# Optimization experiments

Measured on AMD Instinct MI355X. Metric: run time of the kernel, lower is better.

## Reference

```python
import jax, jax.numpy as jnp
import numpy as np

B, S, T, M, H = 16, 128, 1024, 16, 1024
HID = 1024        # attention MLP hidden
WIDTH_EMB = 20    # width embedding dim
N_LING = 2        # len(linguistic_feature_types)


def setup_inputs() -> dict:
    key = jax.random.key(0)
    ks = jax.random.split(key, 12)
    doc_embeddings = jax.random.normal(ks[0], (B, T, H), dtype=jnp.float32)
    start_mappings = jax.random.normal(ks[1], (B, S, T), dtype=jnp.float32)
    end_mappings = jax.random.normal(ks[2], (B, S, T), dtype=jnp.float32)
    continuous_mappings = jax.random.normal(ks[3], (B, S, M, T), dtype=jnp.float32)
    width = jax.random.randint(ks[4], (B, S), 0, M, dtype=jnp.int64)
    linguistic_labels = jax.random.normal(ks[5], (B, S, N_LING), dtype=jnp.float32)
    # attention MLP params (torch Linear layout transposed to x @ W + b)
    W1 = jax.random.normal(ks[6], (H, HID), dtype=jnp.float32) * (1.0 / np.sqrt(H))
    b1 = jax.random.normal(ks[7], (HID,), dtype=jnp.float32) * 0.01
    W2 = jax.random.normal(ks[8], (HID, 1), dtype=jnp.float32) * (1.0 / np.sqrt(HID))
    b2 = jax.random.normal(ks[9], (1,), dtype=jnp.float32) * 0.01
    width_table = jax.random.normal(ks[10], (5, WIDTH_EMB), dtype=jnp.float32)
    return {
        'doc_embeddings': doc_embeddings,
        'start_mappings': start_mappings,
        'end_mappings': end_mappings,
        'continuous_mappings': continuous_mappings,
        'linguistic_labels': linguistic_labels,
        'W1': W1, 'b1': b1, 'W2': W2, 'b2': b2,
        'width_table': width_table,
        'width': width,
    }


def reference(doc_embeddings, start_mappings, end_mappings, continuous_mappings,
              linguistic_labels, W1, b1, W2, b2, width_table, width):
    # one-hot matmul gathers
    start = jnp.einsum('bst,bth->bsh', start_mappings, doc_embeddings)
    end = jnp.einsum('bst,bth->bsh', end_mappings, doc_embeddings)
    cont = jnp.einsum('bsmt,bth->bsmh', continuous_mappings, doc_embeddings)
    b, s, m, h = cont.shape
    vector = jnp.concatenate([start, end], axis=-1).reshape(b * s, 2 * h)
    cont = cont.reshape(b * s, m, h)
    w = width.reshape(b * s)
    ling = linguistic_labels.reshape(b * s, -1)
    # padded masked attention pooling
    masks = (jnp.arange(m)[None, :] < jnp.maximum(w, 1)[:, None]).astype(cont.dtype)
    hdn = jax.nn.relu(jnp.einsum('nmh,hk->nmk', cont, W1) + b1)
    scores = (jnp.einsum('nmk,ko->nmo', hdn, W2) + b2)[..., 0]  # [n, m]
    scores = scores * masks
    scores = jnp.where(scores != 0, scores, jnp.asarray(-9e9, scores.dtype))
    att = jax.nn.softmax(scores, axis=1)
    weighted_sum = jnp.einsum('nm,nmh->nh', att, cont)
    vector = jnp.concatenate([vector, weighted_sum], axis=1)
    # linguistic feature columns (loop over fixed small feature list)
    for fi in range(N_LING):
        vector = jnp.concatenate([vector, ling[:, fi:fi + 1]], axis=1)
    # width embedding (clamp max=4)
    wemb = width_table[jnp.clip(w, 0, 4)]
    vector = jnp.concatenate([vector, wemb], axis=1)
    return vector.reshape(b, s, -1)
```

## Files before the change

kernel.cpp:

```cpp
#include <hip/hip_runtime.h>

typedef unsigned short ushort_t;
typedef unsigned int uint_t;
typedef _Float16 f16;
typedef f16 f16x8 __attribute__((ext_vector_type(8)));
typedef float f32x4 __attribute__((ext_vector_type(4)));

#define B_   16
#define S_   128
#define T_   1024
#define M_   16
#define H_   1024
#define OUTW 3094
#define NSPAN (B_*S_)
#define NROW  (NSPAN*M_)

#define WS_CONT   0
#define WS_DOCT   67108864
#define WS_W1T    100663296
#define WS_SCORES 102760448

__device__ __forceinline__ float sane(float v) {
  return fminf(fmaxf(v, -60000.f), 60000.f);
}
__device__ __forceinline__ ushort_t f16bits(float f) {
  union { f16 h; ushort_t u; } c; c.h = (f16)f; return c.u;
}
__device__ __forceinline__ void load_lds16(const void* g, void* l) {
  __builtin_amdgcn_global_load_lds(
      (const __attribute__((address_space(1))) uint_t*)g,
      (__attribute__((address_space(3))) uint_t*)l, 16, 0, 0);
}

__global__ __launch_bounds__(256) void tconv(const float* __restrict__ in,
                                             ushort_t* __restrict__ out,
                                             int R, int C) {
  __shared__ uint_t tile[64][65];
  const int tid = threadIdx.x;
  const int c0 = blockIdx.x * 64, r0 = blockIdx.y * 64;
  const size_t mo = (size_t)blockIdx.z * R * C;
  const float* ip = in + mo;
  ushort_t* op = out + mo;
  const int tx = tid & 63, ty = tid >> 6;
#pragma unroll
  for (int p = 0; p < 16; ++p) {
    int r = p * 4 + ty;
    tile[r][tx] = (uint_t)f16bits(ip[(size_t)(r0 + r) * C + c0 + tx]);
  }
  __syncthreads();
  const int rr = (tid & 31) * 2, cc0 = tid >> 5;
  uint_t* op32 = (uint_t*)op;
#pragma unroll
  for (int p = 0; p < 8; ++p) {
    int c = cc0 + p * 8;
    uint_t lo = tile[rr][c] & 0xffffu;
    uint_t hi = tile[rr + 1][c] & 0xffffu;
    op32[((size_t)(c0 + c) * R + r0 + rr) >> 1] = lo | (hi << 16);
  }
}

__global__ __launch_bounds__(256) void gemm1(const float* __restrict__ startm,
                                             const float* __restrict__ endm,
                                             const float* __restrict__ contm,
                                             const ushort_t* __restrict__ docT,
                                             float* __restrict__ out,
                                             f16* __restrict__ contF) {
  __shared__ f16 As[2 * 128 * 32];
  __shared__ f16 Bs[2 * 128 * 32];
  const int tid = threadIdx.x;
  const uint_t pid = blockIdx.x;
  const int xcd = pid & 7;
  const int s_  = pid >> 3;
  const int ct  = s_ & 7;
  const int pg  = (s_ >> 3) * 8 + xcd;
  const int rt  = pg >> 4;
  const int b   = pg & 15;

  const float* Ap;
  if (rt == 0)      Ap = startm + (size_t)b * S_ * T_;
  else if (rt == 1) Ap = endm + (size_t)b * S_ * T_;
  else              Ap = contm + (size_t)b * (S_ * M_ * T_) + (size_t)(rt - 2) * 128 * T_;
  const ushort_t* Bp = docT + (size_t)b * (H_ * T_) + (size_t)ct * 128 * T_;

  const int lane = tid & 63, w = tid >> 6;
  const int wr = w >> 1, wc = w & 1;
  const int quad = lane >> 4, l16 = lane & 15;
  const int arow = tid >> 1;
  const int ah   = tid & 1;
  const int asw  = (arow >> 1) & 3;
  const int ac0  = ((2 * ah) ^ asw) * 8;
  const int ac1  = ((2 * ah + 1) ^ asw) * 8;
  const float* aSrc = Ap + (size_t)arow * T_ + ah * 16;
  const int brow = lane >> 2;
  const int bcol = ((lane & 3) ^ ((lane >> 3) & 3)) * 8;

  f32x4 acc[4][4];
#pragma unroll
  for (int i = 0; i < 4; ++i)
#pragma unroll
    for (int j = 0; j < 4; ++j) acc[i][j] = (f32x4){0.f, 0.f, 0.f, 0.f};

  {
    f32x4 a0 = *(const f32x4*)(aSrc + 0);
    f32x4 a1 = *(const f32x4*)(aSrc + 4);
    f32x4 a2 = *(const f32x4*)(aSrc + 8);
    f32x4 a3 = *(const f32x4*)(aSrc + 12);
#pragma unroll
    for (int i = 0; i < 2; ++i) {
      const int rb = w * 32 + i * 16;
      load_lds16(Bp + (size_t)(rb + brow) * T_ + bcol, &Bs[rb * 32]);
    }
    f16x8 h0, h1;
#pragma unroll
    for (int k = 0; k < 4; ++k) {
      h0[k] = (f16)a0[k]; h0[k + 4] = (f16)a1[k];
      h1[k] = (f16)a2[k]; h1[k + 4] = (f16)a3[k];
    }
    *(f16x8*)&As[arow * 32 + ac0] = h0;
    *(f16x8*)&As[arow * 32 + ac1] = h1;
    __syncthreads();
  }

  int cur = 0;
  for (int k0 = 0; k0 < T_; k0 += 32) {
    const int nxt = cur ^ 1;
    const bool pf = (k0 + 32 < T_);
    f32x4 a0, a1, a2, a3;
    if (pf) {
      const float* ap = aSrc + (k0 + 32);
      a0 = *(const f32x4*)(ap + 0);
      a1 = *(const f32x4*)(ap + 4);
      a2 = *(const f32x4*)(ap + 8);
      a3 = *(const f32x4*)(ap + 12);
#pragma unroll
      for (int i = 0; i < 2; ++i) {
        const int rb = w * 32 + i * 16;
        load_lds16(Bp + (size_t)(rb + brow) * T_ + (k0 + 32) + bcol,
                   &Bs[nxt * 4096 + rb * 32]);
      }
    }
    f16x8 af[4], bfr[4];
#pragma unroll
    for (int i = 0; i < 4; ++i) {
      const int row = wr * 64 + i * 16 + l16;
      const int sw = (row >> 1) & 3;
      af[i] = *(const f16x8*)&As[cur * 4096 + row * 32 + ((quad ^ sw) * 8)];
    }
#pragma unroll
    for (int j = 0; j < 4; ++j) {
      const int row = wc * 64 + j * 16 + l16;
      const int sw = (row >> 1) & 3;
      bfr[j] = *(const f16x8*)&Bs[cur * 4096 + row * 32 + ((quad ^ sw) * 8)];
    }
#pragma unroll
    for (int i = 0; i < 4; ++i)
#pragma unroll
      for (int j = 0; j < 4; ++j)
        acc[i][j] = __builtin_amdgcn_mfma_f32_16x16x32_f16(af[i], bfr[j], acc[i][j], 0, 0, 0);
    if (pf) {
      f16x8 h0, h1;
#pragma unroll
      for (int k = 0; k < 4; ++k) {
        h0[k] = (f16)a0[k]; h0[k + 4] = (f16)a1[k];
        h1[k] = (f16)a2[k]; h1[k + 4] = (f16)a3[k];
      }
      *(f16x8*)&As[nxt * 4096 + arow * 32 + ac0] = h0;
      *(f16x8*)&As[nxt * 4096 + arow * 32 + ac1] = h1;
    }
    __syncthreads();
    cur = nxt;
  }

  if (rt < 2) {
    float* op = out + (size_t)b * S_ * OUTW + (size_t)rt * 1024 + (size_t)ct * 128;
#pragma unroll
    for (int i = 0; i < 4; ++i)
#pragma unroll
      for (int j = 0; j < 4; ++j)
#pragma unroll
        for (int r = 0; r < 4; ++r) {
          int row = wr * 64 + i * 16 + quad * 4 + r;
          int col = wc * 64 + j * 16 + l16;
          op[(size_t)row * OUTW + col] = sane(acc[i][j][r]);
        }
  } else {
    f16* cp = contF + ((size_t)b * 2048 + (size_t)(rt - 2) * 128) * H_ + (size_t)ct * 128;
#pragma unroll
    for (int i = 0; i < 4; ++i)
#pragma unroll
      for (int j = 0; j < 4; ++j)
#pragma unroll
        for (int r = 0; r < 4; ++r) {
          int row = wr * 64 + i * 16 + quad * 4 + r;
          int col = wc * 64 + j * 16 + l16;
          cp[(size_t)row * H_ + col] = (f16)sane(acc[i][j][r]);
        }
  }
}

__global__ __launch_bounds__(512) void gemm2(const f16* __restrict__ contF,
                                             const f16* __restrict__ W1T,
                                             const float* __restrict__ b1,
                                             const float* __restrict__ W2,
                                             float* __restrict__ scores) {
  __shared__ f16 As[3][256 * 64];
  __shared__ f16 Bs[3][128 * 64];
  const int tid = threadIdx.x;
  const uint_t pid = blockIdx.x;
  const int xcd = pid & 7;
  const int s_  = pid >> 3;
  const int ct  = s_ & 7;
  const int g   = s_ >> 3;
  const int rt  = g * 8 + xcd;

  const f16* Ap = contF + (size_t)rt * 256 * H_;
  const f16* Bp = W1T + (size_t)ct * 128 * H_;

  const int lane = tid & 63, w = tid >> 6;
  const int wm = w >> 1;
  const int wn = w & 1;
  const int quad = lane >> 4, l16 = lane & 15;
  const int lrow = lane >> 3;
  const int lchk = lane & 7;

  f32x4 acc[4][4];
#pragma unroll
  for (int i = 0; i < 4; ++i)
#pragma unroll
    for (int j = 0; j < 4; ++j) acc[i][j] = (f32x4){0.f, 0.f, 0.f, 0.f};

#pragma unroll
  for (int t = 0; t < 2; ++t) {
    const int k0 = t * 64;
#pragma unroll
    for (int j = 0; j < 4; ++j) {
      const int rowb = w * 32 + j * 8;
      const int row  = rowb + lrow;
      const int c    = lchk ^ (row & 7);
      load_lds16(Ap + (size_t)row * H_ + k0 + c * 8, &As[t][rowb * 64]);
    }
#pragma unroll
    for (int j = 0; j < 2; ++j) {
      const int rowb = w * 16 + j * 8;
      const int row  = rowb + lrow;
      const int c    = lchk ^ (row & 7);
      load_lds16(Bp + (size_t)row * H_ + k0 + c * 8, &Bs[t][rowb * 64]);
    }
  }
  asm volatile("s_waitcnt vmcnt(0)" ::: "memory");
  __syncthreads();

  for (int kt = 0; kt < 16; ++kt) {
    const int rb = kt % 3;
    if (kt + 2 < 16) {
      const int sb = (kt + 2) % 3;
      const int k0 = (kt + 2) * 64;
#pragma unroll
      for (int j = 0; j < 4; ++j) {
        const int rowb = w * 32 + j * 8;
        const int row  = rowb + lrow;
        const int c    = lchk ^ (row & 7);
        load_lds16(Ap + (size_t)row * H_ + k0 + c * 8, &As[sb][rowb * 64]);
      }
#pragma unroll
      for (int j = 0; j < 2; ++j) {
        const int rowb = w * 16 + j * 8;
        const int row  = rowb + lrow;
        const int c    = lchk ^ (row & 7);
        load_lds16(Bp + (size_t)row * H_ + k0 + c * 8, &Bs[sb][rowb * 64]);
      }
    }
    f16x8 af[2][4], bf[2][4];
#pragma unroll
    for (int ks = 0; ks < 2; ++ks) {
#pragma unroll
      for (int mf = 0; mf < 4; ++mf) {
        const int row = wm * 64 + mf * 16 + l16;
        const int c   = ks * 4 + quad;
        af[ks][mf] = *(const f16x8*)&As[rb][row * 64 + ((c ^ (row & 7)) * 8)];
      }
#pragma unroll
      for (int nf = 0; nf < 4; ++nf) {
        const int row = wn * 64 + nf * 16 + l16;
        const int c   = ks * 4 + quad;
        bf[ks][nf] = *(const f16x8*)&Bs[rb][row * 64 + ((c ^ (row & 7)) * 8)];
      }
    }
#pragma unroll
    for (int ks = 0; ks < 2; ++ks)
#pragma unroll
      for (int mf = 0; mf < 4; ++mf)
#pragma unroll
        for (int nf = 0; nf < 4; ++nf)
          acc[mf][nf] = __builtin_amdgcn_mfma_f32_16x16x32_f16(
              af[ks][mf], bf[ks][nf], acc[mf][nf], 0, 0, 0);
    if (kt <= 13) asm volatile("s_waitcnt vmcnt(6) lgkmcnt(0)" ::: "memory");
    else          asm volatile("s_waitcnt vmcnt(0) lgkmcnt(0)" ::: "memory");
    __builtin_amdgcn_s_barrier();
    __builtin_amdgcn_sched_barrier(0);
  }

  const int colbase = ct * 128 + wn * 64;
#pragma unroll
  for (int mf = 0; mf < 4; ++mf) {
#pragma unroll
    for (int r = 0; r < 4; ++r) {
      float t = 0.f;
#pragma unroll
      for (int nf = 0; nf < 4; ++nf) {
        int c = colbase + nf * 16 + l16;
        float v = acc[mf][nf][r] + b1[c];
        v = fmaxf(v, 0.f);
        t = fmaf(v, W2[c], t);
      }
      t += __shfl_xor(t, 1);
      t += __shfl_xor(t, 2);
      t += __shfl_xor(t, 4);
      t += __shfl_xor(t, 8);
      if (l16 == 0) {
        int row = rt * 256 + wm * 64 + mf * 16 + quad * 4 + r;
        atomicAdd(&scores[row], t);
      }
    }
  }
}

__global__ __launch_bounds__(256) void finalize(const f16* __restrict__ contF,
                                                const float* __restrict__ scores,
                                                const float* __restrict__ ling,
                                                const float* __restrict__ b2,
                                                const float* __restrict__ wtab,
                                                const int* __restrict__ width,
                                                float* __restrict__ out) {
  const int n = blockIdx.x;
  const int tid = threadIdx.x;
  __shared__ float sc[16];
  if (tid < 16) {
    float raw = scores[n * 16 + tid] + b2[0];
    if (raw != raw) raw = 0.0f;
    int wv = width[n];
    int wm = wv > 1 ? wv : 1;
    float s = (tid < wm) ? raw : 0.0f;
    if (s == 0.0f) s = -9e9f;
    sc[tid] = s;
  }
  __syncthreads();
  float mx = sc[0];
#pragma unroll
  for (int m = 1; m < 16; ++m) mx = fmaxf(mx, sc[m]);
  float e[16];
  float ssum = 0.f;
#pragma unroll
  for (int m = 0; m < 16; ++m) { e[m] = __expf(sc[m] - mx); ssum += e[m]; }
  const float inv = 1.0f / ssum;
  const f16* cp = contF + (size_t)n * (M_ * H_);
  float* op = out + (size_t)n * OUTW;
#pragma unroll
  for (int hh = 0; hh < 4; ++hh) {
    int h = tid + hh * 256;
    float a = 0.f;
#pragma unroll
    for (int m = 0; m < 16; ++m) a = fmaf(e[m], (float)cp[m * H_ + h], a);
    op[2048 + h] = sane(a * inv);
  }
  if (tid < 2) op[3072 + tid] = ling[n * 2 + tid];
  if (tid < 20) {
    int wv = width[n];
    int wcl = wv < 4 ? wv : 4;
    if (wcl < 0) wcl = 0;
    op[3074 + tid] = wtab[wcl * 20 + tid];
  }
}

extern "C" void kernel_launch(void* const* d_in, const int* in_sizes, int n_in,
                              void* d_out, int out_size, void* d_ws, size_t ws_size,
                              hipStream_t stream) {
  const float* doc    = (const float*)d_in[0];
  const float* startm = (const float*)d_in[1];
  const float* endm   = (const float*)d_in[2];
  const float* contm  = (const float*)d_in[3];
  const float* ling   = (const float*)d_in[4];
  const float* W1     = (const float*)d_in[5];
  const float* b1     = (const float*)d_in[6];
  const float* W2     = (const float*)d_in[7];
  const float* b2     = (const float*)d_in[8];
  const float* wtab   = (const float*)d_in[9];
  const int*   width  = (const int*)d_in[10];
  float* out = (float*)d_out;

  char* ws = (char*)d_ws;
  f16*      contF  = (f16*)(ws + WS_CONT);
  ushort_t* docT   = (ushort_t*)(ws + WS_DOCT);
  f16*      W1T    = (f16*)(ws + WS_W1T);
  float*    scores = (float*)(ws + WS_SCORES);

  hipMemsetAsync(scores, 0, NROW * sizeof(float), stream);
  tconv<<<dim3(16, 16, 16), 256, 0, stream>>>(doc, docT, 1024, 1024);
  tconv<<<dim3(16, 16, 1), 256, 0, stream>>>(W1, (ushort_t*)W1T, 1024, 1024);
  gemm1<<<dim3(2304, 1, 1), 256, 0, stream>>>(startm, endm, contm, docT, out, contF);
  gemm2<<<dim3(1024, 1, 1), 512, 0, stream>>>(contF, (const f16*)W1T, b1, W2, scores);
  finalize<<<dim3(NSPAN, 1, 1), 256, 0, stream>>>(contF, scores, ling, b2, wtab, width, out);
}
```

Measured before the change: 522.8 us.

## Deepen gemm1 prefetch to a triple-buffered B pipeline with explicit waitcnt

```diff
diff --git a/kernel.cpp b/kernel.cpp
--- a/kernel.cpp
+++ b/kernel.cpp
@@ -59,14 +59,66 @@
   }
 }
 
-__global__ __launch_bounds__(256) void gemm1(const float* __restrict__ startm,
-                                             const float* __restrict__ endm,
-                                             const float* __restrict__ contm,
-                                             const ushort_t* __restrict__ docT,
-                                             float* __restrict__ out,
-                                             f16* __restrict__ contF) {
-  __shared__ f16 As[2 * 128 * 32];
-  __shared__ f16 Bs[2 * 128 * 32];
+__device__ __forceinline__ void g1_step(
+    int kk, const float* __restrict__ aSrc, const ushort_t* __restrict__ Bp,
+    f16*& aRd, f16*& aWr, f16*& bRd, f16*& bMid, f16*& bWr,
+    f32x4& P0, f32x4& P1, f32x4& P2, f32x4& P3,
+    f32x4& Q0, f32x4& Q1, f32x4& Q2, f32x4& Q3,
+    f32x4 (&acc)[4][4],
+    int w, int brow, int bcol, int arow, int ac0, int ac1,
+    int wr, int wc, int quad, int l16) {
+  const float* ap = aSrc + kk + 64;
+  Q0 = *(const f32x4*)(ap + 0);
+  Q1 = *(const f32x4*)(ap + 4);
+  Q2 = *(const f32x4*)(ap + 8);
+  Q3 = *(const f32x4*)(ap + 12);
+#pragma unroll
+  for (int i = 0; i < 2; ++i) {
+    const int rb = w * 32 + i * 16;
+    load_lds16(Bp + (size_t)(rb + brow) * T_ + kk + 64 + bcol, bWr + rb * 32);
+  }
+  f16x8 af[4], bfr[4];
+#pragma unroll
+  for (int i = 0; i < 4; ++i) {
+    const int row = wr * 64 + i * 16 + l16;
+    const int sw = (row >> 1) & 3;
+    af[i] = *(const f16x8*)(aRd + row * 32 + ((quad ^ sw) * 8));
+  }
+#pragma unroll
+  for (int j = 0; j < 4; ++j) {
+    const int row = wc * 64 + j * 16 + l16;
+    const int sw = (row >> 1) & 3;
+    bfr[j] = *(const f16x8*)(bRd + row * 32 + ((quad ^ sw) * 8));
+  }
+#pragma unroll
+  for (int i = 0; i < 4; ++i)
+#pragma unroll
+    for (int j = 0; j < 4; ++j)
+      acc[i][j] = __builtin_amdgcn_mfma_f32_16x16x32_f16(af[i], bfr[j], acc[i][j], 0, 0, 0);
+  asm volatile("s_waitcnt vmcnt(6)" ::: "memory");
+  f16x8 h0, h1;
+#pragma unroll
+  for (int k = 0; k < 4; ++k) {
+    h0[k] = (f16)P0[k]; h0[k + 4] = (f16)P1[k];
+    h1[k] = (f16)P2[k]; h1[k + 4] = (f16)P3[k];
+  }
+  *(f16x8*)(aWr + arow * 32 + ac0) = h0;
+  *(f16x8*)(aWr + arow * 32 + ac1) = h1;
+  asm volatile("s_waitcnt lgkmcnt(0)" ::: "memory");
+  __builtin_amdgcn_s_barrier();
+  __builtin_amdgcn_sched_barrier(0);
+  { f16* t = aRd; aRd = aWr; aWr = t; }
+  { f16* t = bRd; bRd = bMid; bMid = bWr; bWr = t; }
+}
+
+__global__ __launch_bounds__(256, 4) void gemm1(const float* __restrict__ startm,
+                                                const float* __restrict__ endm,
+                                                const float* __restrict__ contm,
+                                                const ushort_t* __restrict__ docT,
+                                                float* __restrict__ out,
+                                                f16* __restrict__ contF) {
+  __shared__ f16 As0[128 * 32], As1[128 * 32];
+  __shared__ f16 Bs0[128 * 32], Bs1[128 * 32], Bs2[128 * 32];
   const int tid = threadIdx.x;
   const uint_t pid = blockIdx.x;
   const int xcd = pid & 7;
@@ -100,75 +152,107 @@
 #pragma unroll
     for (int j = 0; j < 4; ++j) acc[i][j] = (f32x4){0.f, 0.f, 0.f, 0.f};
 
+  f16* aRd = As0; f16* aWr = As1;
+  f16* bRd = Bs0; f16* bMid = Bs1; f16* bWr = Bs2;
+  f32x4 P0, P1, P2, P3, Q0, Q1, Q2, Q3;
+
   {
-    f32x4 a0 = *(const f32x4*)(aSrc + 0);
-    f32x4 a1 = *(const f32x4*)(aSrc + 4);
-    f32x4 a2 = *(const f32x4*)(aSrc + 8);
-    f32x4 a3 = *(const f32x4*)(aSrc + 12);
+    f32x4 r0 = *(const f32x4*)(aSrc + 0);
+    f32x4 r1 = *(const f32x4*)(aSrc + 4);
+    f32x4 r2 = *(const f32x4*)(aSrc + 8);
+    f32x4 r3 = *(const f32x4*)(aSrc + 12);
 #pragma unroll
     for (int i = 0; i < 2; ++i) {
       const int rb = w * 32 + i * 16;
-      load_lds16(Bp + (size_t)(rb + brow) * T_ + bcol, &Bs[rb * 32]);
-    }
+      load_lds16(Bp + (size_t)(rb + brow) * T_ + bcol, bRd + rb * 32);
+    }
+    P0 = *(const f32x4*)(aSrc + 32);
+    P1 = *(const f32x4*)(aSrc + 36);
+    P2 = *(const f32x4*)(aSrc + 40);
+    P3 = *(const f32x4*)(aSrc + 44);
+#pragma unroll
+    for (int i = 0; i < 2; ++i) {
+      const int rb = w * 32 + i * 16;
+      load_lds16(Bp + (size_t)(rb + brow) * T_ + 32 + bcol, bMid + rb * 32);
+    }
+    asm volatile("s_waitcnt vmcnt(6)" ::: "memory");
     f16x8 h0, h1;
 #pragma unroll
     for (int k = 0; k < 4; ++k) {
-      h0[k] = (f16)a0[k]; h0[k + 4] = (f16)a1[k];
-      h1[k] = (f16)a2[k]; h1[k + 4] = (f16)a3[k];
-    }
-    *(f16x8*)&As[arow * 32 + ac0] = h0;
-    *(f16x8*)&As[arow * 32 + ac1] = h1;
-    __syncthreads();
-  }
-
-  int cur = 0;
-  for (int k0 = 0; k0 < T_; k0 += 32) {
-    const int nxt = cur ^ 1;
-    const bool pf = (k0 + 32 < T_);
-    f32x4 a0, a1, a2, a3;
-    if (pf) {
-      const float* ap = aSrc + (k0 + 32);
-      a0 = *(const f32x4*)(ap + 0);
-      a1 = *(const f32x4*)(ap + 4);
-      a2 = *(const f32x4*)(ap + 8);
-      a3 = *(const f32x4*)(ap + 12);
-#pragma unroll
-      for (int i = 0; i < 2; ++i) {
-        const int rb = w * 32 + i * 16;
-        load_lds16(Bp + (size_t)(rb + brow) * T_ + (k0 + 32) + bcol,
-                   &Bs[nxt * 4096 + rb * 32]);
-      }
-    }
+      h0[k] = (f16)r0[k]; h0[k + 4] = (f16)r1[k];
+      h1[k] = (f16)r2[k]; h1[k + 4] = (f16)r3[k];
+    }
+    *(f16x8*)(aRd + arow * 32 + ac0) = h0;
+    *(f16x8*)(aRd + arow * 32 + ac1) = h1;
+    asm volatile("s_waitcnt lgkmcnt(0)" ::: "memory");
+    __builtin_amdgcn_s_barrier();
+    __builtin_amdgcn_sched_barrier(0);
+  }
+
+  int kk = 0;
+#pragma unroll 1
+  for (int it = 0; it < 15; ++it) {
+    g1_step(kk, aSrc, Bp, aRd, aWr, bRd, bMid, bWr,
+            P0, P1, P2, P3, Q0, Q1, Q2, Q3, acc,
+            w, brow, bcol, arow, ac0, ac1, wr, wc, quad, l16);
+    kk += 32;
+    g1_step(kk, aSrc, Bp, aRd, aWr, bRd, bMid, bWr,
+            Q0, Q1, Q2, Q3, P0, P1, P2, P3, acc,
+            w, brow, bcol, arow, ac0, ac1, wr, wc, quad, l16);
+    kk += 32;
+  }
+
+  {
     f16x8 af[4], bfr[4];
 #pragma unroll
     for (int i = 0; i < 4; ++i) {
       const int row = wr * 64 + i * 16 + l16;
       const int sw = (row >> 1) & 3;
-      af[i] = *(const f16x8*)&As[cur * 4096 + row * 32 + ((quad ^ sw) * 8)];
+      af[i] = *(const f16x8*)(aRd + row * 32 + ((quad ^ sw) * 8));
     }
 #pragma unroll
     for (int j = 0; j < 4; ++j) {
       const int row = wc * 64 + j * 16 + l16;
       const int sw = (row >> 1) & 3;
-      bfr[j] = *(const f16x8*)&Bs[cur * 4096 + row * 32 + ((quad ^ sw) * 8)];
+      bfr[j] = *(const f16x8*)(bRd + row * 32 + ((quad ^ sw) * 8));
     }
 #pragma unroll
     for (int i = 0; i < 4; ++i)
 #pragma unroll
       for (int j = 0; j < 4; ++j)
         acc[i][j] = __builtin_amdgcn_mfma_f32_16x16x32_f16(af[i], bfr[j], acc[i][j], 0, 0, 0);
-    if (pf) {
-      f16x8 h0, h1;
-#pragma unroll
-      for (int k = 0; k < 4; ++k) {
-        h0[k] = (f16)a0[k]; h0[k + 4] = (f16)a1[k];
-        h1[k] = (f16)a2[k]; h1[k + 4] = (f16)a3[k];
-      }
-      *(f16x8*)&As[nxt * 4096 + arow * 32 + ac0] = h0;
-      *(f16x8*)&As[nxt * 4096 + arow * 32 + ac1] = h1;
-    }
-    __syncthreads();
-    cur = nxt;
+    asm volatile("s_waitcnt vmcnt(0)" ::: "memory");
+    f16x8 h0, h1;
+#pragma unroll
+    for (int k = 0; k < 4; ++k) {
+      h0[k] = (f16)P0[k]; h0[k + 4] = (f16)P1[k];
+      h1[k] = (f16)P2[k]; h1[k + 4] = (f16)P3[k];
+    }
+    *(f16x8*)(aWr + arow * 32 + ac0) = h0;
+    *(f16x8*)(aWr + arow * 32 + ac1) = h1;
+    asm volatile("s_waitcnt lgkmcnt(0)" ::: "memory");
+    __builtin_amdgcn_s_barrier();
+    __builtin_amdgcn_sched_barrier(0);
+  }
+  {
+    f16x8 af[4], bfr[4];
+#pragma unroll
+    for (int i = 0; i < 4; ++i) {
+      const int row = wr * 64 + i * 16 + l16;
+      const int sw = (row >> 1) & 3;
+      af[i] = *(const f16x8*)(aWr + row * 32 + ((quad ^ sw) * 8));
+    }
+#pragma unroll
+    for (int j = 0; j < 4; ++j) {
+      const int row = wc * 64 + j * 16 + l16;
+      const int sw = (row >> 1) & 3;
+      bfr[j] = *(const f16x8*)(bMid + row * 32 + ((quad ^ sw) * 8));
+    }
+#pragma unroll
+    for (int i = 0; i < 4; ++i)
+#pragma unroll
+      for (int j = 0; j < 4; ++j)
+        acc[i][j] = __builtin_amdgcn_mfma_f32_16x16x32_f16(af[i], bfr[j], acc[i][j], 0, 0, 0);
   }
 
   if (rt < 2) {
```

New measurement: 558.1 us. 1.07x slower.
